# Performance work log

Measured on AMD Instinct MI355X. Metric: run time of the kernel, lower is better.

The kernel has to match this reference:

```python
import jax, jax.numpy as jnp
import numpy as np

BASE_SIZE = 16
FEAT_STRIDE = 16


def _generate_anchors(base_size=BASE_SIZE, ratios=np.array([0.5, 1.0, 2.0]), scales=np.array([8.0, 16.0, 32.0])):
    def whctrs(a):
        w = a[2] - a[0] + 1.0
        h = a[3] - a[1] + 1.0
        return w, h, a[0] + 0.5 * (w - 1.0), a[1] + 0.5 * (h - 1.0)

    def mkanchors(ws, hs, xc, yc):
        ws = ws[:, None]
        hs = hs[:, None]
        return np.hstack([xc - 0.5 * (ws - 1.0), yc - 0.5 * (hs - 1.0),
                          xc + 0.5 * (ws - 1.0), yc + 0.5 * (hs - 1.0)])

    base = np.array([1.0, 1.0, base_size, base_size]) - 1.0
    w, h, xc, yc = whctrs(base)
    size = w * h
    ws = np.round(np.sqrt(size / ratios))
    hs = np.round(ws * ratios)
    ratio_anchors = mkanchors(ws, hs, xc, yc)
    out = []
    for ra in ratio_anchors:
        rw, rh, rxc, ryc = whctrs(ra)
        out.append(mkanchors(rw * scales, rh * scales, rxc, ryc))
    return np.vstack(out).astype(np.float32)  # [9, 4]


def setup_inputs() -> dict:
    B, G, H, W = 8, 128, 64, 64
    key = jax.random.key(0)
    k1, k2, k3, k4 = jax.random.split(key, 4)
    rpn_cls_score = jax.random.normal(k1, (B, 2, H, W), dtype=jnp.float32)
    # realistic gt boxes inside a 1024x1024 image, last 32 rows zero-padded
    x1 = jax.random.uniform(k2, (B, G, 1), minval=0.0, maxval=800.0)
    y1 = jax.random.uniform(k3, (B, G, 1), minval=0.0, maxval=800.0)
    wh = jax.random.uniform(k4, (B, G, 2), minval=16.0, maxval=200.0)
    x2 = jnp.clip(x1 + wh[..., 0:1], 0.0, 1023.0)
    y2 = jnp.clip(y1 + wh[..., 1:2], 0.0, 1023.0)
    cls = jnp.ones((B, G, 1), jnp.float32)
    gt = jnp.concatenate([x1, y1, x2, y2, cls], axis=-1)
    valid = (jnp.arange(G) < 96)[None, :, None]
    gt_boxes = jnp.where(valid, gt, 0.0).astype(jnp.float32)
    im_info = jnp.tile(jnp.array([[1024.0, 1024.0, 1.0]], jnp.float32), (B, 1))
    num_boxes = jnp.full((B,), 96, jnp.int32)
    anchors = jnp.asarray(_generate_anchors())
    return {"rpn_cls_score": rpn_cls_score, "gt_boxes": gt_boxes,
            "im_info": im_info, "num_boxes": num_boxes, "anchors": anchors}


def reference(rpn_cls_score, gt_boxes, im_info, num_boxes, anchors):
    H, W = rpn_cls_score.shape[2], rpn_cls_score.shape[3]
    # shift grid over feature map locations -> [K, 4]
    sx = jnp.arange(W, dtype=jnp.float32) * FEAT_STRIDE
    sy = jnp.arange(H, dtype=jnp.float32) * FEAT_STRIDE
    SX, SY = jnp.meshgrid(sx, sy)
    shifts = jnp.stack([SX.ravel(), SY.ravel(), SX.ravel(), SY.ravel()], axis=1)
    all_anchors = (anchors[None, :, :] + shifts[:, None, :]).reshape(-1, 4)  # [K*A, 4]
    im_h, im_w = im_info[0, 0], im_info[0, 1]
    # inside-image filter (allowed_border = 0); expressed as a mask (jit-friendly)
    inside = ((all_anchors[:, 0] >= 0.0) & (all_anchors[:, 1] >= 0.0)
              & (all_anchors[:, 2] < im_w) & (all_anchors[:, 3] < im_h))
    gt = gt_boxes[:, :, :4]  # [B, G, 4]
    aw = all_anchors[:, 2] - all_anchors[:, 0] + 1.0
    ah = all_anchors[:, 3] - all_anchors[:, 1] + 1.0
    a_area = aw * ah  # [N]
    gw = gt[:, :, 2] - gt[:, :, 0] + 1.0
    gh = gt[:, :, 3] - gt[:, :, 1] + 1.0
    g_area = gw * gh  # [B, G]
    # pairwise intersection [B, N, G]
    ix1 = jnp.maximum(all_anchors[None, :, None, 0], gt[:, None, :, 0])
    iy1 = jnp.maximum(all_anchors[None, :, None, 1], gt[:, None, :, 1])
    ix2 = jnp.minimum(all_anchors[None, :, None, 2], gt[:, None, :, 2])
    iy2 = jnp.minimum(all_anchors[None, :, None, 3], gt[:, None, :, 3])
    iw = jnp.maximum(ix2 - ix1 + 1.0, 0.0)
    ih = jnp.maximum(iy2 - iy1 + 1.0, 0.0)
    inter = iw * ih
    ua = a_area[None, :, None] + g_area[:, None, :] - inter
    overlaps = inter / ua
    # zero-area handling as in bbox_overlaps_batch
    gt_zero = (gw == 1.0) & (gh == 1.0)
    a_zero = (aw == 1.0) & (ah == 1.0)
    overlaps = jnp.where(gt_zero[:, None, :], 0.0, overlaps)
    overlaps = jnp.where(a_zero[None, :, None], -1.0, overlaps)
    # mark out-of-image anchors (original gathers inds_inside; we mask densely)
    overlaps = jnp.where(inside[None, :, None], overlaps, -1.0)
    return overlaps
```

## Files before the change

### kernel.cpp

```cpp
#include <hip/hip_runtime.h>

constexpr int G_BOX = 128;
constexpr int N_A   = 9;
constexpr int FW    = 64;
constexpr int FH    = 64;
constexpr int KTOT  = FW * FH * N_A;
constexpr int KPB   = 32;
constexpr int KPT   = 4;

__global__ __launch_bounds__(256) void overlaps_kernel(
    const float* __restrict__ gt_boxes,
    const float* __restrict__ im_info,
    const float* __restrict__ anchors,
    float* __restrict__ out)
{
    __shared__ float s_gx1[G_BOX], s_gy1[G_BOX], s_gx2p[G_BOX], s_gy2p[G_BOX];
    __shared__ float s_garea[G_BOX], s_gnz[G_BOX];
    __shared__ float s_anc[N_A * 4];

    const int t = threadIdx.x;
    const int b = blockIdx.y;

    if (t < G_BOX) {
        const float* gp = gt_boxes + ((size_t)b * G_BOX + t) * 5;
        float x1 = gp[0], y1 = gp[1], x2 = gp[2], y2 = gp[3];
        float gw = x2 - x1 + 1.0f;
        float gh = y2 - y1 + 1.0f;
        s_gx1[t] = x1;
        s_gy1[t] = y1;
        s_gx2p[t] = x2 + 1.0f;
        s_gy2p[t] = y2 + 1.0f;
        s_garea[t] = gw * gh;
        s_gnz[t] = ((gw == 1.0f) && (gh == 1.0f)) ? 0.0f : 1.0f;
    }
    if (t < N_A * 4) s_anc[t] = anchors[t];
    __syncthreads();

    const float im_h = im_info[0];
    const float im_w = im_info[1];

    const int lane_g = t & 31;
    const int kgrp   = t >> 5;
    const int k0     = blockIdx.x * KPB + kgrp * KPT;

    float ax1[KPT], ay1[KPT], ax2p[KPT], ay2p[KPT], aarea[KPT];
    bool  sel[KPT];
    #pragma unroll
    for (int q = 0; q < KPT; ++q) {
        unsigned k = (unsigned)(k0 + q);
        unsigned a = k % 9u;
        unsigned s = k / 9u;
        float sxv = (float)((s & 63u) * 16u);
        float syv = (float)((s >> 6) * 16u);
        float x1 = s_anc[a * 4 + 0] + sxv;
        float y1 = s_anc[a * 4 + 1] + syv;
        float x2 = s_anc[a * 4 + 2] + sxv;
        float y2 = s_anc[a * 4 + 3] + syv;
        float aw = x2 - x1 + 1.0f;
        float ah = y2 - y1 + 1.0f;
        ax1[q] = x1;
        ay1[q] = y1;
        ax2p[q] = x2 + 1.0f;
        ay2p[q] = y2 + 1.0f;
        aarea[q] = aw * ah;
        bool a_zero = (aw == 1.0f) && (ah == 1.0f);
        bool inside = (x1 >= 0.0f) && (y1 >= 0.0f) && (x2 < im_w) && (y2 < im_h);
        sel[q] = a_zero || !inside;
    }

    float* outb = out + (size_t)b * KTOT * G_BOX;

    #pragma unroll
    for (int c = 0; c < 4; ++c) {
        int g = c * 32 + lane_g;
        float gx1 = s_gx1[g], gy1 = s_gy1[g];
        float gx2p = s_gx2p[g], gy2p = s_gy2p[g];
        float garea = s_garea[g], gnz = s_gnz[g];
        #pragma unroll
        for (int q = 0; q < KPT; ++q) {
            float ix1  = fmaxf(ax1[q], gx1);
            float iy1  = fmaxf(ay1[q], gy1);
            float ix2p = fminf(ax2p[q], gx2p);
            float iy2p = fminf(ay2p[q], gy2p);
            float iw = fmaxf(ix2p - ix1, 0.0f);
            float ih = fmaxf(iy2p - iy1, 0.0f);
            float inter = iw * ih;
            float ua = aarea[q] + garea - inter;
            float v = inter * __builtin_amdgcn_rcpf(ua);
            v *= gnz;
            v = sel[q] ? -1.0f : v;
            outb[(size_t)(k0 + q) * G_BOX + g] = v;
        }
    }
}

extern "C" void kernel_launch(void* const* d_in, const int* in_sizes, int n_in,
                              void* d_out, int out_size, void* d_ws, size_t ws_size,
                              hipStream_t stream) {
    const float* gt_boxes = (const float*)d_in[1];
    const float* im_info  = (const float*)d_in[2];
    const float* anchors  = (const float*)d_in[4];
    float* out = (float*)d_out;

    dim3 grid(KTOT / KPB, 8);
    dim3 block(256);
    overlaps_kernel<<<grid, block, 0, stream>>>(gt_boxes, im_info, anchors, out);
}
```

Measured before the change: 28.52 us.

## Assign four consecutive gt boxes per lane and store float4 rows

```diff
diff --git a/kernel.cpp b/kernel.cpp
--- a/kernel.cpp
+++ b/kernel.cpp
@@ -2,11 +2,10 @@
 
 constexpr int G_BOX = 128;
 constexpr int N_A   = 9;
-constexpr int FW    = 64;
-constexpr int FH    = 64;
-constexpr int KTOT  = FW * FH * N_A;
-constexpr int KPB   = 32;
-constexpr int KPT   = 4;
+constexpr int KTOT  = 64 * 64 * N_A;
+constexpr int KPQ   = 8;
+constexpr int NKG   = 8;
+constexpr int KPB   = KPQ * NKG;
 
 __global__ __launch_bounds__(256) void overlaps_kernel(
     const float* __restrict__ gt_boxes,
@@ -14,8 +13,7 @@
     const float* __restrict__ anchors,
     float* __restrict__ out)
 {
-    __shared__ float s_gx1[G_BOX], s_gy1[G_BOX], s_gx2p[G_BOX], s_gy2p[G_BOX];
-    __shared__ float s_garea[G_BOX], s_gnz[G_BOX];
+    __shared__ float s_g[G_BOX][6];
     __shared__ float s_anc[N_A * 4];
 
     const int t = threadIdx.x;
@@ -26,12 +24,12 @@
         float x1 = gp[0], y1 = gp[1], x2 = gp[2], y2 = gp[3];
         float gw = x2 - x1 + 1.0f;
         float gh = y2 - y1 + 1.0f;
-        s_gx1[t] = x1;
-        s_gy1[t] = y1;
-        s_gx2p[t] = x2 + 1.0f;
-        s_gy2p[t] = y2 + 1.0f;
-        s_garea[t] = gw * gh;
-        s_gnz[t] = ((gw == 1.0f) && (gh == 1.0f)) ? 0.0f : 1.0f;
+        s_g[t][0] = x1;
+        s_g[t][1] = y1;
+        s_g[t][2] = x2 + 1.0f;
+        s_g[t][3] = y2 + 1.0f;
+        s_g[t][4] = gw * gh;
+        s_g[t][5] = ((gw == 1.0f) && (gh == 1.0f)) ? 0.0f : 1.0f;
     }
     if (t < N_A * 4) s_anc[t] = anchors[t];
     __syncthreads();
@@ -39,14 +37,22 @@
     const float im_h = im_info[0];
     const float im_w = im_info[1];
 
-    const int lane_g = t & 31;
-    const int kgrp   = t >> 5;
-    const int k0     = blockIdx.x * KPB + kgrp * KPT;
+    const int lane = t & 31;
+    const int kgrp = t >> 5;
+    const int k0   = blockIdx.x * KPB + kgrp * KPQ;
 
-    float ax1[KPT], ay1[KPT], ax2p[KPT], ay2p[KPT], aarea[KPT];
-    bool  sel[KPT];
+    float gx1[4], gy1[4], gx2p[4], gy2p[4], garea[4], gnz[4];
     #pragma unroll
-    for (int q = 0; q < KPT; ++q) {
+    for (int j = 0; j < 4; ++j) {
+        const float* sg = s_g[4 * lane + j];
+        gx1[j] = sg[0]; gy1[j] = sg[1]; gx2p[j] = sg[2];
+        gy2p[j] = sg[3]; garea[j] = sg[4]; gnz[j] = sg[5];
+    }
+
+    float* outp = out + (((size_t)b * KTOT + k0) * G_BOX + 4 * lane);
+
+    #pragma unroll
+    for (int q = 0; q < KPQ; ++q) {
         unsigned k = (unsigned)(k0 + q);
         unsigned a = k % 9u;
         unsigned s = k / 9u;
@@ -58,39 +64,30 @@
         float y2 = s_anc[a * 4 + 3] + syv;
         float aw = x2 - x1 + 1.0f;
         float ah = y2 - y1 + 1.0f;
-        ax1[q] = x1;
-        ay1[q] = y1;
-        ax2p[q] = x2 + 1.0f;
-        ay2p[q] = y2 + 1.0f;
-        aarea[q] = aw * ah;
+        float ax2p = x2 + 1.0f;
+        float ay2p = y2 + 1.0f;
+        float aarea = aw * ah;
         bool a_zero = (aw == 1.0f) && (ah == 1.0f);
         bool inside = (x1 >= 0.0f) && (y1 >= 0.0f) && (x2 < im_w) && (y2 < im_h);
-        sel[q] = a_zero || !inside;
-    }
+        bool sel = a_zero || !inside;
 
-    float* outb = out + (size_t)b * KTOT * G_BOX;
-
-    #pragma unroll
-    for (int c = 0; c < 4; ++c) {
-        int g = c * 32 + lane_g;
-        float gx1 = s_gx1[g], gy1 = s_gy1[g];
-        float gx2p = s_gx2p[g], gy2p = s_gy2p[g];
-        float garea = s_garea[g], gnz = s_gnz[g];
+        float4 v;
+        float* vp = &v.x;
         #pragma unroll
-        for (int q = 0; q < KPT; ++q) {
-            float ix1  = fmaxf(ax1[q], gx1);
-            float iy1  = fmaxf(ay1[q], gy1);
-            float ix2p = fminf(ax2p[q], gx2p);
-            float iy2p = fminf(ay2p[q], gy2p);
+        for (int j = 0; j < 4; ++j) {
+            float ix1  = fmaxf(x1, gx1[j]);
+            float iy1  = fmaxf(y1, gy1[j]);
+            float ix2p = fminf(ax2p, gx2p[j]);
+            float iy2p = fminf(ay2p, gy2p[j]);
             float iw = fmaxf(ix2p - ix1, 0.0f);
             float ih = fmaxf(iy2p - iy1, 0.0f);
             float inter = iw * ih;
-            float ua = aarea[q] + garea - inter;
-            float v = inter * __builtin_amdgcn_rcpf(ua);
-            v *= gnz;
-            v = sel[q] ? -1.0f : v;
-            outb[(size_t)(k0 + q) * G_BOX + g] = v;
+            float ua = aarea + garea[j] - inter;
+            float r = inter * __builtin_amdgcn_rcpf(ua);
+            r *= gnz[j];
+            vp[j] = sel ? -1.0f : r;
         }
+        *reinterpret_cast<float4*>(outp + (size_t)q * G_BOX) = v;
     }
 }
 
```

Result: no change. 28.79 us (+0.9%).
